# Kernel optimization log

Hardware: AMD Instinct MI355X
Metric: run time of the kernel (lower is better)

The kernel has to match this reference:

```python
import jax, jax.numpy as jnp
import numpy as np


def setup_inputs() -> dict:
    key = jax.random.key(0)
    k1, k2 = jax.random.split(key)
    bs, T, dfeat = 16, 1024, 80
    h = jax.random.normal(k1, (bs, T, dfeat), dtype=jnp.float32)
    d = jax.random.uniform(k2, (bs, T), dtype=jnp.float32)
    sigma = jnp.ones((1,), dtype=jnp.float32)
    size = 4096
    return {"h": h, "d": d, "sigma": sigma, "size": size}


def reference(h, d, sigma, size):
    # cumsum of durations, rolled right by one along T
    cs = jnp.roll(jnp.cumsum(d, axis=1), 1, axis=1)
    # faithful to torch source: cumsum[0] = 0 zeroes the whole first BATCH row
    cs = cs.at[0].set(0.0)
    c = d / 2 + cs                                  # [bs, T] gaussian centers
    two_sigma_sq = 2 * sigma ** 2                   # [1]
    t = jnp.arange(1, size + 1, dtype=jnp.float32) + 0.5  # [size]
    # scores: -(t - c)^2 / (2*sigma^2), shape [bs, size, T]
    scores = -((t[None, :, None] - c[:, None, :]) ** 2) / two_sigma_sq
    W = jax.nn.softmax(scores, axis=-1)             # softmax over T
    u = jnp.einsum('bst,btd->bsd', W, h)            # [bs, size, d]
    return u
```

## Files before the change

kernel.cpp:

```cpp
#include <hip/hip_runtime.h>

#define T      1024
#define DFEAT  80
#define NF4    20
#define NF4P   21
#define CH     160
#define MARGIN 40.0f
#define WIN_S  64
#define B0_SB  8

__global__ void centers_kernel(const float* __restrict__ d, float* __restrict__ c) {
    __shared__ double s[T];
    int b = blockIdx.x;
    int t = threadIdx.x;
    float dv = d[b * T + t];
    s[t] = (double)dv;
    __syncthreads();
    for (int off = 1; off < T; off <<= 1) {
        double add = (t >= off) ? s[t - off] : 0.0;
        __syncthreads();
        s[t] += add;
        __syncthreads();
    }
    double cs;
    if (b == 0)      cs = 0.0;
    else if (t == 0) cs = s[T - 1];
    else             cs = s[t - 1];
    c[b * T + t] = (float)((double)dv * 0.5 + cs);
}

__device__ __forceinline__ int lower_bound_c(const float* cl, float x) {
    int base = 1, len = T - 1;
    while (len > 0) {
        int half = len >> 1;
        if (cl[base + half] < x) { base += half + 1; len -= half + 1; }
        else len = half;
    }
    return base;
}

__global__ __launch_bounds__(256) void win_kernel(
    const float* __restrict__ h, const float* __restrict__ c,
    const float* __restrict__ sigma, float* __restrict__ u, int size)
{
    __shared__ float  cl[T];
    __shared__ float4 hs[CH * NF4P];
    __shared__ float  wred[4];

    const int b   = blockIdx.y + 1;
    const int s0  = blockIdx.x * WIN_S;
    const int tid = threadIdx.x;
    const int sq  = tid >> 2;
    const int q   = tid & 3;
    int s = s0 + sq;
    if (s >= size) s = size - 1;

    for (int i = tid; i < T; i += 256) cl[i] = c[b * T + i];
    __syncthreads();

    const float sg  = sigma[0];
    const float tss = 2.0f * sg * sg;
    const float ts  = (float)s + 1.5f;

    int ins = lower_bound_c(cl, ts);
    float d0 = fabsf(ts - cl[0]);
    if (ins < T) d0 = fminf(d0, fabsf(cl[ins] - ts));
    if (ins > 1) d0 = fminf(d0, fabsf(ts - cl[ins - 1]));
    const float v0  = -(d0 * d0) / tss;
    const float Ws  = sqrtf(fmaf(sg * sg, MARGIN, d0 * d0));
    const int   jlo = lower_bound_c(cl, ts - Ws);
    const int   jhi = lower_bound_c(cl, ts + Ws);

    float wmax = Ws;
    #pragma unroll
    for (int o = 32; o > 0; o >>= 1) wmax = fmaxf(wmax, __shfl_xor(wmax, o));
    if ((tid & 63) == 0) wred[tid >> 6] = wmax;
    __syncthreads();
    wmax = fmaxf(fmaxf(wred[0], wred[1]), fmaxf(wred[2], wred[3]));
    const int rlo = lower_bound_c(cl, (float)s0 + 1.5f - wmax);
    const int rhi = lower_bound_c(cl, (float)(s0 + WIN_S - 1) + 1.5f + wmax);

    float4 acc[5];
    #pragma unroll
    for (int i5 = 0; i5 < 5; ++i5) acc[i5] = make_float4(0.f, 0.f, 0.f, 0.f);
    float lsum = 0.f;

    const float4* hb4 = (const float4*)h + (size_t)b * T * NF4;

    for (int r0 = rlo; r0 < rhi; r0 += CH) {
        const int nr = min(CH, rhi - r0);
        __syncthreads();
        for (int i = tid; i < nr * NF4; i += 256) {
            int row = i / NF4, k = i - row * NF4;
            hs[row * NF4P + k] = hb4[(size_t)(r0 + row) * NF4 + k];
        }
        __syncthreads();
        const int a = max(jlo, r0), e = min(jhi, r0 + nr);
        for (int j = a; j < e; ++j) {
            float dd = ts - cl[j];
            float v  = -(dd * dd) / tss;
            float w  = __expf(v - v0);
            lsum += w;
            const float4* hr = &hs[(j - r0) * NF4P + q];
            #pragma unroll
            for (int i5 = 0; i5 < 5; ++i5) {
                float4 hv = hr[4 * i5];
                acc[i5].x += w * hv.x; acc[i5].y += w * hv.y;
                acc[i5].z += w * hv.z; acc[i5].w += w * hv.w;
            }
        }
    }

    {
        float dd = ts - cl[0];
        if (fabsf(dd) <= Ws) {
            float v = -(dd * dd) / tss;
            float w = __expf(v - v0);
            lsum += w;
            const float4* hr = hb4 + q;
            #pragma unroll
            for (int i5 = 0; i5 < 5; ++i5) {
                float4 hv = hr[4 * i5];
                acc[i5].x += w * hv.x; acc[i5].y += w * hv.y;
                acc[i5].z += w * hv.z; acc[i5].w += w * hv.w;
            }
        }
    }

    const float inv = 1.0f / lsum;
    float4* ur = (float4*)(u + ((size_t)b * size + s) * DFEAT) + q;
    #pragma unroll
    for (int i5 = 0; i5 < 5; ++i5) {
        float4 a4 = acc[i5];
        ur[4 * i5] = make_float4(a4.x * inv, a4.y * inv, a4.z * inv, a4.w * inv);
    }
}

__global__ __launch_bounds__(256) void b0_kernel(
    const float* __restrict__ h, const float* __restrict__ c,
    const float* __restrict__ sigma, float* __restrict__ u, int size)
{
    __shared__ float  cl[T];
    __shared__ float4 hs[CH * NF4P];

    const int tid  = threadIdx.x;
    const int wid  = tid >> 6;
    const int lane = tid & 63;
    const int jsub = lane & 15;
    const int kg   = lane >> 4;
    const int sA   = blockIdx.x * B0_SB + wid * 2;
    const int sB   = sA + 1;

    for (int i = tid; i < T; i += 256) cl[i] = c[i];
    __syncthreads();

    const float sg  = sigma[0];
    const float tss = 2.0f * sg * sg;
    const float tsA = (float)sA + 1.5f;
    const float tsB = (float)sB + 1.5f;

    float dA = 1e30f, dB = 1e30f;
    for (int jj = lane; jj < T; jj += 64) {
        float cv = cl[jj];
        dA = fminf(dA, fabsf(tsA - cv));
        dB = fminf(dB, fabsf(tsB - cv));
    }
    #pragma unroll
    for (int o = 32; o > 0; o >>= 1) {
        dA = fminf(dA, __shfl_xor(dA, o));
        dB = fminf(dB, __shfl_xor(dB, o));
    }
    const float v0A = -(dA * dA) / tss;
    const float v0B = -(dB * dB) / tss;

    float4 accA[5], accB[5];
    #pragma unroll
    for (int i5 = 0; i5 < 5; ++i5) {
        accA[i5] = make_float4(0.f, 0.f, 0.f, 0.f);
        accB[i5] = make_float4(0.f, 0.f, 0.f, 0.f);
    }
    float lsA = 0.f, lsB = 0.f;
    const float4* hb4 = (const float4*)h;

    for (int r0 = 0; r0 < T; r0 += CH) {
        const int nr = min(CH, T - r0);
        __syncthreads();
        for (int i = tid; i < nr * NF4; i += 256) {
            int row = i / NF4, k = i - row * NF4;
            hs[row * NF4P + k] = hb4[(size_t)(r0 + row) * NF4 + k];
        }
        __syncthreads();
        for (int j = r0 + jsub; j < r0 + nr; j += 16) {
            float cv  = cl[j];
            float ddA = tsA - cv, ddB = tsB - cv;
            float vA  = -(ddA * ddA) / tss;
            float vB  = -(ddB * ddB) / tss;
            float wA  = __expf(vA - v0A);
            float wB  = __expf(vB - v0B);
            lsA += wA; lsB += wB;
            const float4* hr = &hs[(j - r0) * NF4P + kg];
            #pragma unroll
            for (int i5 = 0; i5 < 5; ++i5) {
                float4 hv = hr[4 * i5];
                accA[i5].x += wA * hv.x; accA[i5].y += wA * hv.y;
                accA[i5].z += wA * hv.z; accA[i5].w += wA * hv.w;
                accB[i5].x += wB * hv.x; accB[i5].y += wB * hv.y;
                accB[i5].z += wB * hv.z; accB[i5].w += wB * hv.w;
            }
        }
    }

    #pragma unroll
    for (int o = 8; o > 0; o >>= 1) {
        lsA += __shfl_down(lsA, o);
        lsB += __shfl_down(lsB, o);
        #pragma unroll
        for (int i5 = 0; i5 < 5; ++i5) {
            accA[i5].x += __shfl_down(accA[i5].x, o);
            accA[i5].y += __shfl_down(accA[i5].y, o);
            accA[i5].z += __shfl_down(accA[i5].z, o);
            accA[i5].w += __shfl_down(accA[i5].w, o);
            accB[i5].x += __shfl_down(accB[i5].x, o);
            accB[i5].y += __shfl_down(accB[i5].y, o);
            accB[i5].z += __shfl_down(accB[i5].z, o);
            accB[i5].w += __shfl_down(accB[i5].w, o);
        }
    }

    if (jsub == 0) {
        const float invA = 1.0f / lsA, invB = 1.0f / lsB;
        float4* uA = (float4*)(u + (size_t)sA * DFEAT) + kg;
        float4* uB = (float4*)(u + (size_t)sB * DFEAT) + kg;
        #pragma unroll
        for (int i5 = 0; i5 < 5; ++i5) {
            float4 a4 = accA[i5], b4 = accB[i5];
            uA[4 * i5] = make_float4(a4.x * invA, a4.y * invA, a4.z * invA, a4.w * invA);
            uB[4 * i5] = make_float4(b4.x * invB, b4.y * invB, b4.z * invB, b4.w * invB);
        }
    }
}

extern "C" void kernel_launch(void* const* d_in, const int* in_sizes, int n_in,
                              void* d_out, int out_size, void* d_ws, size_t ws_size,
                              hipStream_t stream) {
    const float* h     = (const float*)d_in[0];
    const float* d     = (const float*)d_in[1];
    const float* sigma = (const float*)d_in[2];
    float* u = (float*)d_out;

    int bs   = in_sizes[1] / T;
    int size = out_size / (bs * DFEAT);

    float* c = (float*)d_ws;

    hipLaunchKernelGGL(centers_kernel, dim3(bs), dim3(T), 0, stream, d, c);
    if (bs > 1)
        hipLaunchKernelGGL(win_kernel, dim3((size + WIN_S - 1) / WIN_S, bs - 1),
                           dim3(256), 0, stream, h, c, sigma, u, size);
    hipLaunchKernelGGL(b0_kernel, dim3(size / B0_SB), dim3(256), 0, stream,
                       h, c, sigma, u, size);
}
```

Before: 138.7 us.

## Register-block four rows in b0 kernel, wave-level scan for centers, smaller win chunk

The batch-0 dense kernel now has each wave compute four output positions instead of two. It stores h transposed in shared memory, so one shared load of h is reused across four weight sets, cutting LDS traffic per FMA. The centers prefix sum is rewritten as a single-wave scan: each lane holds 16 values and uses shuffles instead of a 1024-thread block with many barriers. The windowed kernel's staging chunk shrinks from 160 to 96 rows to lower LDS use and raise occupancy. The risks are higher register pressure from 80 accumulators in b0, and b0 launching half as many blocks.

New measurement: 138.0 us. No clear change (-0.5%).

```diff
diff --git a/kernel.cpp b/kernel.cpp
--- a/kernel.cpp
+++ b/kernel.cpp
@@ -4,29 +4,43 @@
 #define DFEAT  80
 #define NF4    20
 #define NF4P   21
-#define CH     160
+#define W_CH   96
 #define MARGIN 40.0f
 #define WIN_S  64
-#define B0_SB  8
-
-__global__ void centers_kernel(const float* __restrict__ d, float* __restrict__ c) {
-    __shared__ double s[T];
-    int b = blockIdx.x;
-    int t = threadIdx.x;
-    float dv = d[b * T + t];
-    s[t] = (double)dv;
-    __syncthreads();
-    for (int off = 1; off < T; off <<= 1) {
-        double add = (t >= off) ? s[t - off] : 0.0;
-        __syncthreads();
-        s[t] += add;
-        __syncthreads();
-    }
-    double cs;
-    if (b == 0)      cs = 0.0;
-    else if (t == 0) cs = s[T - 1];
-    else             cs = s[t - 1];
-    c[b * T + t] = (float)((double)dv * 0.5 + cs);
+#define B0_CH  128
+#define B0_ST  133
+
+__global__ __launch_bounds__(64) void centers_kernel(
+    const float* __restrict__ d, float* __restrict__ c)
+{
+    const int b = blockIdx.x, lane = threadIdx.x;
+    const float4* dr4 = (const float4*)(d + (size_t)b * T) + lane * 4;
+    float4 a0 = dr4[0], a1 = dr4[1], a2 = dr4[2], a3 = dr4[3];
+    float loc[16] = {a0.x,a0.y,a0.z,a0.w, a1.x,a1.y,a1.z,a1.w,
+                     a2.x,a2.y,a2.z,a2.w, a3.x,a3.y,a3.z,a3.w};
+    double pre[17];
+    pre[0] = 0.0;
+    #pragma unroll
+    for (int i = 0; i < 16; ++i) pre[i + 1] = pre[i] + (double)loc[i];
+    const double lsum = pre[16];
+    double x = lsum;
+    #pragma unroll
+    for (int off = 1; off < 64; off <<= 1) {
+        double y = __shfl_up(x, off);
+        if (lane >= off) x += y;
+    }
+    const double exclb = x - lsum;
+    const double total = __shfl(x, 63);
+    const int t0 = lane * 16;
+    #pragma unroll
+    for (int i = 0; i < 16; ++i) {
+        int t = t0 + i;
+        double cs;
+        if (b == 0)      cs = 0.0;
+        else if (t == 0) cs = total;
+        else             cs = exclb + pre[i];
+        c[(size_t)b * T + t] = (float)((double)loc[i] * 0.5 + cs);
+    }
 }
 
 __device__ __forceinline__ int lower_bound_c(const float* cl, float x) {
@@ -44,7 +58,7 @@
     const float* __restrict__ sigma, float* __restrict__ u, int size)
 {
     __shared__ float  cl[T];
-    __shared__ float4 hs[CH * NF4P];
+    __shared__ float4 hs[W_CH * NF4P];
     __shared__ float  wred[4];
 
     const int b   = blockIdx.y + 1;
@@ -55,7 +69,7 @@
     int s = s0 + sq;
     if (s >= size) s = size - 1;
 
-    for (int i = tid; i < T; i += 256) cl[i] = c[b * T + i];
+    for (int i = tid; i < T; i += 256) cl[i] = c[(size_t)b * T + i];
     __syncthreads();
 
     const float sg  = sigma[0];
@@ -87,8 +101,8 @@
 
     const float4* hb4 = (const float4*)h + (size_t)b * T * NF4;
 
-    for (int r0 = rlo; r0 < rhi; r0 += CH) {
-        const int nr = min(CH, rhi - r0);
+    for (int r0 = rlo; r0 < rhi; r0 += W_CH) {
+        const int nr = min(W_CH, rhi - r0);
         __syncthreads();
         for (int i = tid; i < nr * NF4; i += 256) {
             int row = i / NF4, k = i - row * NF4;
@@ -141,101 +155,100 @@
     const float* __restrict__ sigma, float* __restrict__ u, int size)
 {
     __shared__ float  cl[T];
-    __shared__ float4 hs[CH * NF4P];
-
-    const int tid  = threadIdx.x;
-    const int wid  = tid >> 6;
-    const int lane = tid & 63;
-    const int jsub = lane & 15;
-    const int kg   = lane >> 4;
-    const int sA   = blockIdx.x * B0_SB + wid * 2;
-    const int sB   = sA + 1;
+    __shared__ float4 hsT[NF4 * B0_ST];
+
+    const int tid   = threadIdx.x;
+    const int wid   = tid >> 6;
+    const int lane  = tid & 63;
+    const int kg    = lane >> 4;
+    const int jsub  = lane & 15;
+    const int sbase = blockIdx.x * 16 + wid * 4;
 
     for (int i = tid; i < T; i += 256) cl[i] = c[i];
     __syncthreads();
 
     const float sg  = sigma[0];
     const float tss = 2.0f * sg * sg;
-    const float tsA = (float)sA + 1.5f;
-    const float tsB = (float)sB + 1.5f;
-
-    float dA = 1e30f, dB = 1e30f;
+    float ts[4];
+    #pragma unroll
+    for (int q = 0; q < 4; ++q) ts[q] = (float)(sbase + q) + 1.5f;
+
+    float dm[4] = {1e30f, 1e30f, 1e30f, 1e30f};
     for (int jj = lane; jj < T; jj += 64) {
         float cv = cl[jj];
-        dA = fminf(dA, fabsf(tsA - cv));
-        dB = fminf(dB, fabsf(tsB - cv));
-    }
-    #pragma unroll
-    for (int o = 32; o > 0; o >>= 1) {
-        dA = fminf(dA, __shfl_xor(dA, o));
-        dB = fminf(dB, __shfl_xor(dB, o));
-    }
-    const float v0A = -(dA * dA) / tss;
-    const float v0B = -(dB * dB) / tss;
-
-    float4 accA[5], accB[5];
-    #pragma unroll
-    for (int i5 = 0; i5 < 5; ++i5) {
-        accA[i5] = make_float4(0.f, 0.f, 0.f, 0.f);
-        accB[i5] = make_float4(0.f, 0.f, 0.f, 0.f);
-    }
-    float lsA = 0.f, lsB = 0.f;
+        #pragma unroll
+        for (int q = 0; q < 4; ++q) dm[q] = fminf(dm[q], fabsf(ts[q] - cv));
+    }
+    #pragma unroll
+    for (int o = 32; o > 0; o >>= 1)
+        #pragma unroll
+        for (int q = 0; q < 4; ++q) dm[q] = fminf(dm[q], __shfl_xor(dm[q], o));
+    float v0[4];
+    #pragma unroll
+    for (int q = 0; q < 4; ++q) v0[q] = -(dm[q] * dm[q]) / tss;
+
+    float4 acc[4][5];
+    #pragma unroll
+    for (int q = 0; q < 4; ++q)
+        #pragma unroll
+        for (int i5 = 0; i5 < 5; ++i5) acc[q][i5] = make_float4(0.f, 0.f, 0.f, 0.f);
+    float ls[4] = {0.f, 0.f, 0.f, 0.f};
+
     const float4* hb4 = (const float4*)h;
-
-    for (int r0 = 0; r0 < T; r0 += CH) {
-        const int nr = min(CH, T - r0);
-        __syncthreads();
-        for (int i = tid; i < nr * NF4; i += 256) {
+    for (int r0 = 0; r0 < T; r0 += B0_CH) {
+        __syncthreads();
+        for (int i = tid; i < B0_CH * NF4; i += 256) {
             int row = i / NF4, k = i - row * NF4;
-            hs[row * NF4P + k] = hb4[(size_t)(r0 + row) * NF4 + k];
-        }
-        __syncthreads();
-        for (int j = r0 + jsub; j < r0 + nr; j += 16) {
-            float cv  = cl[j];
-            float ddA = tsA - cv, ddB = tsB - cv;
-            float vA  = -(ddA * ddA) / tss;
-            float vB  = -(ddB * ddB) / tss;
-            float wA  = __expf(vA - v0A);
-            float wB  = __expf(vB - v0B);
-            lsA += wA; lsB += wB;
-            const float4* hr = &hs[(j - r0) * NF4P + kg];
-            #pragma unroll
-            for (int i5 = 0; i5 < 5; ++i5) {
-                float4 hv = hr[4 * i5];
-                accA[i5].x += wA * hv.x; accA[i5].y += wA * hv.y;
-                accA[i5].z += wA * hv.z; accA[i5].w += wA * hv.w;
-                accB[i5].x += wB * hv.x; accB[i5].y += wB * hv.y;
-                accB[i5].z += wB * hv.z; accB[i5].w += wB * hv.w;
+            hsT[k * B0_ST + row] = hb4[(size_t)(r0 + row) * NF4 + k];
+        }
+        __syncthreads();
+        for (int j = jsub; j < B0_CH; j += 16) {
+            float cv = cl[r0 + j];
+            float w[4];
+            #pragma unroll
+            for (int q = 0; q < 4; ++q) {
+                float dd = ts[q] - cv;
+                float v  = -(dd * dd) / tss;
+                w[q] = __expf(v - v0[q]);
+                ls[q] += w[q];
+            }
+            #pragma unroll
+            for (int i5 = 0; i5 < 5; ++i5) {
+                float4 hv = hsT[(kg + 4 * i5) * B0_ST + j];
+                #pragma unroll
+                for (int q = 0; q < 4; ++q) {
+                    acc[q][i5].x += w[q] * hv.x; acc[q][i5].y += w[q] * hv.y;
+                    acc[q][i5].z += w[q] * hv.z; acc[q][i5].w += w[q] * hv.w;
+                }
             }
         }
     }
 
     #pragma unroll
     for (int o = 8; o > 0; o >>= 1) {
-        lsA += __shfl_down(lsA, o);
-        lsB += __shfl_down(lsB, o);
-        #pragma unroll
-        for (int i5 = 0; i5 < 5; ++i5) {
-            accA[i5].x += __shfl_down(accA[i5].x, o);
-            accA[i5].y += __shfl_down(accA[i5].y, o);
-            accA[i5].z += __shfl_down(accA[i5].z, o);
-            accA[i5].w += __shfl_down(accA[i5].w, o);
-            accB[i5].x += __shfl_down(accB[i5].x, o);
-            accB[i5].y += __shfl_down(accB[i5].y, o);
-            accB[i5].z += __shfl_down(accB[i5].z, o);
-            accB[i5].w += __shfl_down(accB[i5].w, o);
+        #pragma unroll
+        for (int q = 0; q < 4; ++q) {
+            ls[q] += __shfl_down(ls[q], o);
+            #pragma unroll
+            for (int i5 = 0; i5 < 5; ++i5) {
+                acc[q][i5].x += __shfl_down(acc[q][i5].x, o);
+                acc[q][i5].y += __shfl_down(acc[q][i5].y, o);
+                acc[q][i5].z += __shfl_down(acc[q][i5].z, o);
+                acc[q][i5].w += __shfl_down(acc[q][i5].w, o);
+            }
         }
     }
 
     if (jsub == 0) {
-        const float invA = 1.0f / lsA, invB = 1.0f / lsB;
-        float4* uA = (float4*)(u + (size_t)sA * DFEAT) + kg;
-        float4* uB = (float4*)(u + (size_t)sB * DFEAT) + kg;
-        #pragma unroll
-        for (int i5 = 0; i5 < 5; ++i5) {
-            float4 a4 = accA[i5], b4 = accB[i5];
-            uA[4 * i5] = make_float4(a4.x * invA, a4.y * invA, a4.z * invA, a4.w * invA);
-            uB[4 * i5] = make_float4(b4.x * invB, b4.y * invB, b4.z * invB, b4.w * invB);
+        #pragma unroll
+        for (int q = 0; q < 4; ++q) {
+            const float inv = 1.0f / ls[q];
+            float4* ur = (float4*)(u + (size_t)(sbase + q) * DFEAT) + kg;
+            #pragma unroll
+            for (int i5 = 0; i5 < 5; ++i5) {
+                float4 a4 = acc[q][i5];
+                ur[4 * i5] = make_float4(a4.x * inv, a4.y * inv, a4.z * inv, a4.w * inv);
+            }
         }
     }
 }
@@ -253,10 +266,10 @@
 
     float* c = (float*)d_ws;
 
-    hipLaunchKernelGGL(centers_kernel, dim3(bs), dim3(T), 0, stream, d, c);
+    hipLaunchKernelGGL(centers_kernel, dim3(bs), dim3(64), 0, stream, d, c);
     if (bs > 1)
         hipLaunchKernelGGL(win_kernel, dim3((size + WIN_S - 1) / WIN_S, bs - 1),
                            dim3(256), 0, stream, h, c, sigma, u, size);
-    hipLaunchKernelGGL(b0_kernel, dim3(size / B0_SB), dim3(256), 0, stream,
+    hipLaunchKernelGGL(b0_kernel, dim3(size / 16), dim3(256), 0, stream,
                        h, c, sigma, u, size);
 }
```
